# Kernel optimization log

Hardware: AMD Instinct MI355X
Metric: run time of the kernel (lower is better)

## Reference

```python
import jax, jax.numpy as jnp
import numpy as np
from jax import lax

B, T, I, H, L = 512, 2048, 16, 40, 3

def setup_inputs() -> dict:
    key = jax.random.key(0)
    ks = jax.random.split(key, 4 * L + 3)
    bound = 1.0 / np.sqrt(H)
    u = lambda k, shp: jax.random.uniform(k, shp, jnp.float32, -bound, bound)
    inp = {"x": jax.random.normal(ks[0], (B, T, I), jnp.float32)}
    for l in range(L):
        in_dim = I if l == 0 else H
        inp[f"w_ih{l}"] = u(ks[1 + 4 * l], (H, in_dim))
        inp[f"w_hh{l}"] = u(ks[2 + 4 * l], (H, H))
        inp[f"b_ih{l}"] = u(ks[3 + 4 * l], (H,))
        inp[f"b_hh{l}"] = u(ks[4 + 4 * l], (H,))
    inp["fc_w"] = u(ks[4 * L + 1], (1, H))
    inp["fc_b"] = u(ks[4 * L + 2], (1,))
    return inp

def _rnn_layer(x_seq, w_ih, w_hh, b_ih, b_hh):
    # Precompute input projection as one big GEMM: [B, T, H]
    xp = jnp.einsum('bti,hi->bth', x_seq, w_ih) + b_ih + b_hh
    h0 = jnp.zeros((x_seq.shape[0], w_hh.shape[0]), x_seq.dtype)
    def step(h, xt):  # xt: [B, H]
        h = jnp.tanh(xt + h @ w_hh.T)
        return h, h
    _, ys = lax.scan(step, h0, jnp.swapaxes(xp, 0, 1))  # [T, B, H]
    return jnp.swapaxes(ys, 0, 1)  # [B, T, H]

def reference(x, w_ih0, w_hh0, b_ih0, b_hh0,
              w_ih1, w_hh1, b_ih1, b_hh1,
              w_ih2, w_hh2, b_ih2, b_hh2, fc_w, fc_b):
    # Multi-layer tanh RNN (eval mode: inter-layer and final dropout are identity)
    h = _rnn_layer(x, w_ih0, w_hh0, b_ih0, b_hh0)
    h = _rnn_layer(h, w_ih1, w_hh1, b_ih1, b_hh1)
    h = _rnn_layer(h, w_ih2, w_hh2, b_ih2, b_hh2)
    last = h[:, -1, :]                     # [B, H]
    out = last @ fc_w.T + fc_b             # [B, 1]
    return out[:, 0]                       # [B]
```

## Files before the change

kernel.cpp:

```cpp
#include <hip/hip_runtime.h>
#include <cstddef>
#include <cstdint>

#define B_ 512
#define T_ 2048
#define I_ 16
#define H_ 40

typedef __fp16 half_t;
typedef half_t h2 __attribute__((ext_vector_type(2)));
typedef half_t h8 __attribute__((ext_vector_type(8)));

__device__ __forceinline__ float fast_tanh(float x) {
  float e = __builtin_amdgcn_exp2f(x * 2.8853900817779268f);
  return 1.0f - 2.0f * __builtin_amdgcn_rcpf(e + 1.0f);
}

__device__ __forceinline__ float dot2(h2 a, h2 b, float c) {
#if __has_builtin(__builtin_amdgcn_fdot2)
  return __builtin_amdgcn_fdot2(a, b, c, false);
#else
  return c + (float)a[0] * (float)b[0] + (float)a[1] * (float)b[1];
#endif
}

__device__ __forceinline__ h2 pack2(float lo, float hi) {
#if __has_builtin(__builtin_amdgcn_cvt_pkrtz)
  return __builtin_amdgcn_cvt_pkrtz(lo, hi);
#else
  h2 r; r[0] = (half_t)lo; r[1] = (half_t)hi; return r;
#endif
}

#define PIN(v) asm volatile("" : "+v"(v))

#define LOADW(DST, SRC, STR, N2)                                    \
  _Pragma("unroll") for (int k = 0; k < (N2); ++k) {                \
    DST[k][0] = (half_t)SRC[jr * (STR) + 2 * k];                    \
    DST[k][1] = (half_t)SRC[jr * (STR) + 2 * k + 1];                \
    PIN(DST[k]);                                                    \
  }

#define HD(HP, W)                                                   \
  do {                                                              \
    _Pragma("unroll") for (int m = 0; m < 5; ++m) {                 \
      h8 q = (HP)[m];                                               \
      h2 p0 = {q[0], q[1]}, p1 = {q[2], q[3]};                      \
      h2 p2 = {q[4], q[5]}, p3 = {q[6], q[7]};                      \
      a0 = dot2(p0, (W)[4 * m + 0], a0);                            \
      a1 = dot2(p1, (W)[4 * m + 1], a1);                            \
      a2 = dot2(p2, (W)[4 * m + 2], a2);                            \
      a3 = dot2(p3, (W)[4 * m + 3], a3);                            \
    }                                                               \
  } while (0)

#define STEP(XH)                                                    \
  do {                                                              \
    const h8* hp0 = (const h8*)&hb16[0][0];                         \
    const h8* hp1 = (const h8*)&hb16[1][0];                         \
    const h8* hp2 = (const h8*)&hb16[2][0];                         \
                                             \
    float a0 = bias0, a1 = 0.f, a2 = 0.f, a3 = 0.f;                 \
    a0 = dot2(XH[0], w0i[0], a0); a1 = dot2(XH[1], w0i[1], a1);     \
    a2 = dot2(XH[2], w0i[2], a2); a3 = dot2(XH[3], w0i[3], a3);     \
    a0 = dot2(XH[4], w0i[4], a0); a1 = dot2(XH[5], w0i[5], a1);     \
    a2 = dot2(XH[6], w0i[6], a2); a3 = dot2(XH[7], w0i[7], a3);     \
    HD(hp0, w0h);                                       \
    const float nh0 = fast_tanh((a0 + a1) + (a2 + a3));             \
    hb16[0][j] = (half_t)nh0;                                       \
                                             \
    a0 = bias1; a1 = a2 = a3 = 0.f;                                 \
    HD(hp0, w1i);                                       \
    HD(hp1, w1h);                                       \
    const float nh1 = fast_tanh((a0 + a1) + (a2 + a3));             \
    hb16[1][j] = (half_t)nh1;                                       \
                                             \
    a0 = bias2; a1 = a2 = a3 = 0.f;                                 \
    HD(hp1, w2i);                                       \
    HD(hp2, w2h);                                       \
    nh2v = fast_tanh((a0 + a1) + (a2 + a3));                        \
    hb16[2][j] = (half_t)nh2v;                                      \
  } while (0)

__device__ __forceinline__ void loadx(h2* xh, const float* __restrict__ p) {
  float4 f0 = ((const float4*)p)[0];
  float4 f1 = ((const float4*)p)[1];
  float4 f2 = ((const float4*)p)[2];
  float4 f3 = ((const float4*)p)[3];
  xh[0] = pack2(f0.x, f0.y); xh[1] = pack2(f0.z, f0.w);
  xh[2] = pack2(f1.x, f1.y); xh[3] = pack2(f1.z, f1.w);
  xh[4] = pack2(f2.x, f2.y); xh[5] = pack2(f2.z, f2.w);
  xh[6] = pack2(f3.x, f3.y); xh[7] = pack2(f3.z, f3.w);
}

__global__ __launch_bounds__(64)
__attribute__((amdgpu_waves_per_eu(1, 1)))
void rnn3_fused(const float* __restrict__ x,
                const float* __restrict__ wih0, const float* __restrict__ whh0,
                const float* __restrict__ bih0, const float* __restrict__ bhh0,
                const float* __restrict__ wih1, const float* __restrict__ whh1,
                const float* __restrict__ bih1, const float* __restrict__ bhh1,
                const float* __restrict__ wih2, const float* __restrict__ whh2,
                const float* __restrict__ bih2, const float* __restrict__ bhh2,
                const float* __restrict__ fcw, const float* __restrict__ fcb,
                float* __restrict__ out) {
  const int b = blockIdx.x;
  const int j = threadIdx.x;
  const int jr = (j < H_) ? j : (H_ - 1);

  h2 w0i[I_ / 2], w0h[H_ / 2], w1i[H_ / 2], w1h[H_ / 2], w2i[H_ / 2], w2h[H_ / 2];
  LOADW(w0i, wih0, I_, I_ / 2)
  LOADW(w0h, whh0, H_, H_ / 2)
  LOADW(w1i, wih1, H_, H_ / 2)
  LOADW(w1h, whh1, H_, H_ / 2)
  LOADW(w2i, wih2, H_, H_ / 2)
  LOADW(w2h, whh2, H_, H_ / 2)

  float bias0 = bih0[jr] + bhh0[jr]; PIN(bias0);
  float bias1 = bih1[jr] + bhh1[jr]; PIN(bias1);
  float bias2 = bih2[jr] + bhh2[jr]; PIN(bias2);

  __shared__ __align__(16) half_t hb16[3][64];
  hb16[0][j] = (half_t)0.f; hb16[1][j] = (half_t)0.f; hb16[2][j] = (half_t)0.f;
  __syncthreads();

  const float* __restrict__ xb = x + (size_t)b * (T_ * I_);

  h2 xA[8], xB[8];
  loadx(xA, xb);
  loadx(xB, xb + I_);

  float nh2v = 0.f;

  for (int t = 0; t < T_; t += 2) {
    STEP(xA);
    { const int tf = (t + 2 < T_) ? t + 2 : t;     loadx(xA, xb + (size_t)tf * I_); }
    STEP(xB);
    { const int tf = (t + 3 < T_) ? t + 3 : t + 1; loadx(xB, xb + (size_t)tf * I_); }
  }

  const float fw = (j < H_) ? fcw[j] : 0.f;
  float v = nh2v * fw;
#pragma unroll
  for (int off = 32; off > 0; off >>= 1) v += __shfl_down(v, off);
  if (j == 0) out[b] = v + fcb[0];
}

extern "C" void kernel_launch(void* const* d_in, const int* in_sizes, int n_in,
                              void* d_out, int out_size, void* d_ws, size_t ws_size,
                              hipStream_t stream) {
  (void)in_sizes; (void)n_in; (void)d_ws; (void)ws_size; (void)out_size;
  const float* x    = (const float*)d_in[0];
  const float* wih0 = (const float*)d_in[1];
  const float* whh0 = (const float*)d_in[2];
  const float* bih0 = (const float*)d_in[3];
  const float* bhh0 = (const float*)d_in[4];
  const float* wih1 = (const float*)d_in[5];
  const float* whh1 = (const float*)d_in[6];
  const float* bih1 = (const float*)d_in[7];
  const float* bhh1 = (const float*)d_in[8];
  const float* wih2 = (const float*)d_in[9];
  const float* whh2 = (const float*)d_in[10];
  const float* bih2 = (const float*)d_in[11];
  const float* bhh2 = (const float*)d_in[12];
  const float* fcw  = (const float*)d_in[13];
  const float* fcb  = (const float*)d_in[14];
  float* out = (float*)d_out;

  hipLaunchKernelGGL(rnn3_fused, dim3(B_), dim3(64), 0, stream,
                     x, wih0, whh0, bih0, bhh0,
                     wih1, whh1, bih1, bhh1,
                     wih2, whh2, bih2, bhh2,
                     fcw, fcb, out);
}
```

Baseline: 1.102 ms.

## Skew the three RNN layers in time so their updates run in parallel

The layers are now pipelined diagonally. At each tick, layer 0 computes step u, layer 1 computes step u-1 and layer 2 computes step u-2. All hidden states are read from LDS before any are written, so the three dot-product chains and tanh evaluations are independent within a tick. This removes the serial layer-to-layer dependency inside each timestep, which dominated this latency-bound single-wave kernel. Prologue and epilogue ticks fill and drain the pipeline, at the cost of more live registers for the extra accumulators and LDS reads.

```diff
diff --git a/kernel.cpp b/kernel.cpp
--- a/kernel.cpp
+++ b/kernel.cpp
@@ -41,46 +41,53 @@
     PIN(DST[k]);                                                    \
   }
 
-#define HD(HP, W)                                                   \
-  do {                                                              \
-    _Pragma("unroll") for (int m = 0; m < 5; ++m) {                 \
-      h8 q = (HP)[m];                                               \
-      h2 p0 = {q[0], q[1]}, p1 = {q[2], q[3]};                      \
-      h2 p2 = {q[4], q[5]}, p3 = {q[6], q[7]};                      \
-      a0 = dot2(p0, (W)[4 * m + 0], a0);                            \
-      a1 = dot2(p1, (W)[4 * m + 1], a1);                            \
-      a2 = dot2(p2, (W)[4 * m + 2], a2);                            \
-      a3 = dot2(p3, (W)[4 * m + 3], a3);                            \
-    }                                                               \
-  } while (0)
+#define HD4(Q, W, A0, A1, A2, A3)                                   \
+  _Pragma("unroll") for (int m = 0; m < 5; ++m) {                   \
+    h2 p0 = {Q[m][0], Q[m][1]}, p1 = {Q[m][2], Q[m][3]};            \
+    h2 p2 = {Q[m][4], Q[m][5]}, p3 = {Q[m][6], Q[m][7]};            \
+    A0 = dot2(p0, (W)[4 * m + 0], A0);                              \
+    A1 = dot2(p1, (W)[4 * m + 1], A1);                              \
+    A2 = dot2(p2, (W)[4 * m + 2], A2);                              \
+    A3 = dot2(p3, (W)[4 * m + 3], A3);                              \
+  }
 
-#define STEP(XH)                                                    \
-  do {                                                              \
-    const h8* hp0 = (const h8*)&hb16[0][0];                         \
-    const h8* hp1 = (const h8*)&hb16[1][0];                         \
-    const h8* hp2 = (const h8*)&hb16[2][0];                         \
-                                             \
-    float a0 = bias0, a1 = 0.f, a2 = 0.f, a3 = 0.f;                 \
-    a0 = dot2(XH[0], w0i[0], a0); a1 = dot2(XH[1], w0i[1], a1);     \
-    a2 = dot2(XH[2], w0i[2], a2); a3 = dot2(XH[3], w0i[3], a3);     \
-    a0 = dot2(XH[4], w0i[4], a0); a1 = dot2(XH[5], w0i[5], a1);     \
-    a2 = dot2(XH[6], w0i[6], a2); a3 = dot2(XH[7], w0i[7], a3);     \
-    HD(hp0, w0h);                                       \
-    const float nh0 = fast_tanh((a0 + a1) + (a2 + a3));             \
-    hb16[0][j] = (half_t)nh0;                                       \
-                                             \
-    a0 = bias1; a1 = a2 = a3 = 0.f;                                 \
-    HD(hp0, w1i);                                       \
-    HD(hp1, w1h);                                       \
-    const float nh1 = fast_tanh((a0 + a1) + (a2 + a3));             \
-    hb16[1][j] = (half_t)nh1;                                       \
-                                             \
-    a0 = bias2; a1 = a2 = a3 = 0.f;                                 \
-    HD(hp1, w2i);                                       \
-    HD(hp2, w2h);                                       \
-    nh2v = fast_tanh((a0 + a1) + (a2 + a3));                        \
-    hb16[2][j] = (half_t)nh2v;                                      \
-  } while (0)
+#define TICK(D0, D1, D2, XH) do {                                   \
+  h8 q0[5], q1[5], q2[5];                                           \
+  if (D0 || D1) { _Pragma("unroll") for (int m = 0; m < 5; ++m)     \
+      q0[m] = ((const h8*)&hb16[0][0])[m]; }                        \
+  if (D1 || D2) { _Pragma("unroll") for (int m = 0; m < 5; ++m)     \
+      q1[m] = ((const h8*)&hb16[1][0])[m]; }                        \
+  if (D2)       { _Pragma("unroll") for (int m = 0; m < 5; ++m)     \
+      q2[m] = ((const h8*)&hb16[2][0])[m]; }                        \
+  float a0=0.f,a1=0.f,a2=0.f,a3=0.f;                                \
+  float b0=0.f,b1=0.f,b2=0.f,b3=0.f;                                \
+  float c0=0.f,c1=0.f,c2=0.f,c3=0.f;                                \
+  float nh0=0.f, nh1=0.f;                                           \
+  if (D0) {                                                         \
+    a0 = bias0;                                                     \
+    a0=dot2(XH[0],w0i[0],a0); a1=dot2(XH[1],w0i[1],a1);             \
+    a2=dot2(XH[2],w0i[2],a2); a3=dot2(XH[3],w0i[3],a3);             \
+    a0=dot2(XH[4],w0i[4],a0); a1=dot2(XH[5],w0i[5],a1);             \
+    a2=dot2(XH[6],w0i[6],a2); a3=dot2(XH[7],w0i[7],a3);             \
+    HD4(q0, w0h, a0,a1,a2,a3)                          \
+  }                                                                 \
+  if (D1) {                                                         \
+    b0 = bias1;                                                     \
+    HD4(q0, w1i, b0,b1,b2,b3)                          \
+    HD4(q1, w1h, b0,b1,b2,b3)                          \
+  }                                                                 \
+  if (D2) {                                                         \
+    c0 = bias2;                                                     \
+    HD4(q1, w2i, c0,c1,c2,c3)                          \
+    HD4(q2, w2h, c0,c1,c2,c3)                          \
+  }                                                                 \
+  if (D0) nh0  = fast_tanh((a0 + a1) + (a2 + a3));                  \
+  if (D1) nh1  = fast_tanh((b0 + b1) + (b2 + b3));                  \
+  if (D2) nh2v = fast_tanh((c0 + c1) + (c2 + c3));                  \
+  if (D0) hb16[0][j] = (half_t)nh0;                                 \
+  if (D1) hb16[1][j] = (half_t)nh1;                                 \
+  if (D2) hb16[2][j] = (half_t)nh2v;                                \
+} while (0)
 
 __device__ __forceinline__ void loadx(h2* xh, const float* __restrict__ p) {
   float4 f0 = ((const float4*)p)[0];
@@ -99,7 +106,7 @@
                 const float* __restrict__ wih0, const float* __restrict__ whh0,
                 const float* __restrict__ bih0, const float* __restrict__ bhh0,
                 const float* __restrict__ wih1, const float* __restrict__ whh1,
-                const float* __restrict__ bih1, const float* __restrict__ bhh1,
+                const float* __restrict__ b_ih1, const float* __restrict__ bhh1,
                 const float* __restrict__ wih2, const float* __restrict__ whh2,
                 const float* __restrict__ bih2, const float* __restrict__ bhh2,
                 const float* __restrict__ fcw, const float* __restrict__ fcb,
@@ -116,9 +123,9 @@
   LOADW(w2i, wih2, H_, H_ / 2)
   LOADW(w2h, whh2, H_, H_ / 2)
 
-  float bias0 = bih0[jr] + bhh0[jr]; PIN(bias0);
-  float bias1 = bih1[jr] + bhh1[jr]; PIN(bias1);
-  float bias2 = bih2[jr] + bhh2[jr]; PIN(bias2);
+  float bias0 = bih0[jr] + bhh0[jr];  PIN(bias0);
+  float bias1 = b_ih1[jr] + bhh1[jr]; PIN(bias1);
+  float bias2 = bih2[jr] + bhh2[jr];  PIN(bias2);
 
   __shared__ __align__(16) half_t hb16[3][64];
   hb16[0][j] = (half_t)0.f; hb16[1][j] = (half_t)0.f; hb16[2][j] = (half_t)0.f;
@@ -132,12 +139,18 @@
 
   float nh2v = 0.f;
 
-  for (int t = 0; t < T_; t += 2) {
-    STEP(xA);
-    { const int tf = (t + 2 < T_) ? t + 2 : t;     loadx(xA, xb + (size_t)tf * I_); }
-    STEP(xB);
-    { const int tf = (t + 3 < T_) ? t + 3 : t + 1; loadx(xB, xb + (size_t)tf * I_); }
+  TICK(1, 0, 0, xA);  loadx(xA, xb + 2 * I_);
+  TICK(1, 1, 0, xB);  loadx(xB, xb + 3 * I_);
+
+  for (int u = 2; u < T_; u += 2) {
+    TICK(1, 1, 1, xA);
+    { const int tf = (u + 2 < T_) ? u + 2 : T_ - 1; loadx(xA, xb + (size_t)tf * I_); }
+    TICK(1, 1, 1, xB);
+    { const int tf = (u + 3 < T_) ? u + 3 : T_ - 1; loadx(xB, xb + (size_t)tf * I_); }
   }
+
+  TICK(0, 1, 1, xA);
+  TICK(0, 0, 1, xA);
 
   const float fw = (j < H_) ? fcw[j] : 0.f;
   float v = nh2v * fw;
```

Result: no change. 1.109 ms (+0.6%).
